# Optimization experiments

Measured on AMD Instinct MI355X. Metric: run time of the kernel, lower is better.

The kernel has to match this reference:

```python
import jax, jax.numpy as jnp
import numpy as np

EMBED_DIM = 1024
NUM_HEADS = 16
HEAD_DIM = EMBED_DIM // NUM_HEADS
BATCH = 2
SEQ = 2048


def setup_inputs() -> dict:
    key = jax.random.key(0)
    k1, k2, k3, k4, k5 = jax.random.split(key, 5)
    scale_in = 1.0 / np.sqrt(EMBED_DIM)
    return {
        "x": jax.random.normal(k1, (BATCH, SEQ, EMBED_DIM), dtype=jnp.float32),
        "head_mask": jnp.ones((NUM_HEADS,), dtype=jnp.float32),
        "qkv_w": jax.random.normal(k2, (3 * EMBED_DIM, EMBED_DIM), dtype=jnp.float32) * scale_in,
        "qkv_b": jax.random.normal(k3, (3 * EMBED_DIM,), dtype=jnp.float32) * 0.02,
        "fc_w": jax.random.normal(k4, (EMBED_DIM, EMBED_DIM), dtype=jnp.float32) * scale_in,
        "fc_b": jax.random.normal(k5, (EMBED_DIM,), dtype=jnp.float32) * 0.02,
    }


def reference(x, head_mask, qkv_w, qkv_b, fc_w, fc_b):
    N, S, D = x.shape
    H, hd = NUM_HEADS, HEAD_DIM
    # qkv Linear: y = x @ W^T + b -> [N, S, 3D]
    qkv = jnp.einsum("nsd,ed->nse", x, qkv_w) + qkv_b
    # reshape (N, S, H, 3, hd) then permute(3,0,2,1,4) -> (3, N, H, S, hd)
    qkv = qkv.reshape(N, S, H, 3, hd).transpose(3, 0, 2, 1, 4)
    q, k, v = qkv[0], qkv[1], qkv[2]
    hm = head_mask.reshape(1, H, 1, 1)
    q = q * hm
    k = k * hm
    v = v * hm
    # scores [N, H, S, S]
    energy = jnp.einsum("nhqd,nhkd->nhqk", q, k)
    attention = jax.nn.softmax(energy / jnp.sqrt(jnp.float32(hd)), axis=-1)
    out = jnp.einsum("nhqk,nhkd->nhqd", attention, v)
    out = out.transpose(0, 2, 1, 3).reshape(N, S, H * hd)
    out = jnp.einsum("nsd,ed->nse", out, fc_w) + fc_b
    return out
```

## Files before the change

### kernel.cpp

```cpp
#include <hip/hip_runtime.h>
#include <hip/hip_bf16.h>

typedef __bf16 bf16;
typedef __attribute__((ext_vector_type(8))) __bf16 bf16x8;
typedef __attribute__((ext_vector_type(4))) __bf16 bf16x4;
typedef __attribute__((ext_vector_type(4))) float f32x4;
typedef __attribute__((ext_vector_type(4))) unsigned int uint4x;

#if __has_builtin(__builtin_amdgcn_exp2f)
#define EXP2F(x) __builtin_amdgcn_exp2f(x)
#else
#define EXP2F(x) exp2f(x)
#endif

#define AS1 __attribute__((address_space(1)))
#define AS3 __attribute__((address_space(3)))

static __device__ __forceinline__ void async_ld16(const bf16* g, bf16* l) {
  __builtin_amdgcn_global_load_lds((const AS1 void*)g, (AS3 void*)l, 16, 0, 0);
}

static __device__ __forceinline__ unsigned bf16rne(float x) {
  unsigned u = __float_as_uint(x);
  return (u + 0x7fffu + ((u >> 16) & 1u)) >> 16;
}
static __device__ __forceinline__ unsigned pack2(float a, float b) {
  return bf16rne(a) | (bf16rne(b) << 16);
}

__global__ void cvt3_kernel(const float* __restrict__ x, const float* __restrict__ qw,
                            const float* __restrict__ fw, bf16* __restrict__ xb,
                            bf16* __restrict__ qwb, bf16* __restrict__ fwb) {
  int b = blockIdx.x;
  const float* src;
  bf16* dst;
  int i;
  if (b < 4096) { src = x; dst = xb; i = b * 256 + threadIdx.x; }
  else if (b < 7168) { src = qw; dst = qwb; i = (b - 4096) * 256 + threadIdx.x; }
  else { src = fw; dst = fwb; i = (b - 7168) * 256 + threadIdx.x; }
  f32x4 v = *(const f32x4*)(src + (size_t)i * 4);
  bf16x4 o;
  o[0] = (bf16)v[0]; o[1] = (bf16)v[1]; o[2] = (bf16)v[2]; o[3] = (bf16)v[3];
  *(bf16x4*)(dst + (size_t)i * 4) = o;
}

#define GEMM_STAGE(k0_, buf_)                                                    \
  {                                                                              \
    async_ld16(A + (size_t)(rowBase + r0) * Kdim + (k0_) + csw, &As[buf_][f0]);  \
    async_ld16(A + (size_t)(rowBase + r1) * Kdim + (k0_) + csw, &As[buf_][f1]);  \
    async_ld16(Bw + (size_t)(colBase + r0) * Kdim + (k0_) + csw, &Bs[buf_][f0]); \
    async_ld16(Bw + (size_t)(colBase + r1) * Kdim + (k0_) + csw, &Bs[buf_][f1]); \
  }

template <int MODE>
__global__ __launch_bounds__(256, 2) void gemm_bt_kernel(
    const bf16* __restrict__ A, const bf16* __restrict__ Bw,
    const float* __restrict__ bias, const float* __restrict__ hm,
    bf16* __restrict__ Qp, bf16* __restrict__ Kp, bf16* __restrict__ Vp,
    float* __restrict__ outF, int Ncols, int Kdim, int rowBlkCount) {
  __shared__ bf16 As[2][128 * 32];
  __shared__ bf16 Bs[2][128 * 32];
  const int t = threadIdx.x, lane = t & 63, w = t >> 6;
  const int wr = w >> 1, wc = w & 1;
  const int j = lane & 15, quad = lane >> 4;
  const int rowBlk = blockIdx.x % rowBlkCount;
  const int colBlk = blockIdx.x / rowBlkCount;
  const int rowBase = rowBlk * 128, colBase = colBlk * 128;

  f32x4 acc[4][4];
  const f32x4 z4 = {0.f, 0.f, 0.f, 0.f};
#pragma unroll
  for (int i = 0; i < 4; ++i)
#pragma unroll
    for (int jj = 0; jj < 4; ++jj) acc[i][jj] = z4;

  const int f0 = t * 8;
  const int f1 = f0 + 2048;
  const int r0 = f0 >> 5, r1 = r0 + 64;
  const int csw = (((t & 3) ^ ((r0 >> 1) & 3))) * 8;
  const int qsw = (quad ^ ((j >> 1) & 3)) * 8;

  GEMM_STAGE(0, 0);
  int buf = 0;
  for (int k0 = 0; k0 < Kdim; k0 += 32) {
    __syncthreads();
    if (k0 + 32 < Kdim) GEMM_STAGE(k0 + 32, buf ^ 1);
    bf16x8 af[4], bfr[4];
#pragma unroll
    for (int i = 0; i < 4; ++i)
      af[i] = *(const bf16x8*)&As[buf][(wr * 64 + i * 16 + j) * 32 + qsw];
#pragma unroll
    for (int jj = 0; jj < 4; ++jj)
      bfr[jj] = *(const bf16x8*)&Bs[buf][(wc * 64 + jj * 16 + j) * 32 + qsw];
#pragma unroll
    for (int i = 0; i < 4; ++i)
#pragma unroll
      for (int jj = 0; jj < 4; ++jj)
        acc[i][jj] = __builtin_amdgcn_mfma_f32_16x16x32_bf16(af[i], bfr[jj], acc[i][jj], 0, 0, 0);
    buf ^= 1;
  }

  if (MODE == 0) {
#pragma unroll
    for (int jj = 0; jj < 4; ++jj) {
      int col = colBase + wc * 64 + jj * 16 + j;
      int hh = col / 192;
      int rem = col - hh * 192;
      int mm = rem >> 6;
      int dd = rem & 63;
      float hmv = hm[hh];
      float bv = bias[col];
      float sc = (mm == 0) ? hmv * 0.18033688011112042f : hmv;
#pragma unroll
      for (int i = 0; i < 4; ++i) {
#pragma unroll
        for (int r = 0; r < 4; ++r) {
          int row = rowBase + wr * 64 + i * 16 + quad * 4 + r;
          int n = row >> 11, ss = row & 2047;
          size_t nh = (size_t)(n * 16 + hh);
          float val = (acc[i][jj][r] + bv) * sc;
          if (mm == 0) {
            Qp[nh * 131072 + ss * 64 + dd] = (bf16)val;
          } else if (mm == 1) {
            size_t idx = nh * 131072 + (size_t)(ss >> 7) * 8192 +
                         (size_t)(2 * ((ss >> 5) & 3) + ((ss >> 2) & 1)) * 1024 +
                         (dd >> 5) * 512 + ((dd >> 3) & 3) * 128 +
                         (((ss >> 3) & 3) * 4 + (ss & 3)) * 8 + (dd & 7);
            Kp[idx] = (bf16)val;
          } else {
            size_t idx = nh * 131072 + (size_t)(ss >> 7) * 8192 +
                         (((ss >> 5) & 3) * 4 + (dd >> 4)) * 512 +
                         ((ss >> 3) & 3) * 128 + (dd & 15) * 8 + (ss & 7);
            Vp[idx] = (bf16)val;
          }
        }
      }
    }
  } else {
#pragma unroll
    for (int jj = 0; jj < 4; ++jj) {
      int col = colBase + wc * 64 + jj * 16 + j;
      float bv = bias[col];
#pragma unroll
      for (int i = 0; i < 4; ++i)
#pragma unroll
        for (int r = 0; r < 4; ++r) {
          int row = rowBase + wr * 64 + i * 16 + quad * 4 + r;
          outF[(size_t)row * Ncols + col] = acc[i][jj][r] + bv;
        }
    }
  }
}

#define FLASH_STAGE(tileIdx, KsBuf, VsBuf)                                  \
  {                                                                         \
    const bf16* kn_ = Kc + (tileIdx) * 4096;                                \
    const bf16* vn_ = Vc + (tileIdx) * 4096;                                \
    _Pragma("unroll")                                                       \
    for (int p = 0; p < 2; ++p) {                                           \
      int c = (p * 256 + t) * 8;                                            \
      async_ld16(kn_ + c, &KsBuf[c]);                                       \
      async_ld16(vn_ + c, &VsBuf[c]);                                       \
    }                                                                       \
  }

#define FLASH_TILE(KsBuf, VsBuf)                                            \
  {                                                                         \
    unsigned pkd[2][4][2];                                                  \
    _Pragma("unroll")                                                       \
    for (int ct = 0; ct < 4; ++ct) {                                        \
      bf16x8 kf0 = *(const bf16x8*)&KsBuf[ct * 1024 + lane * 8];            \
      bf16x8 kf1 = *(const bf16x8*)&KsBuf[ct * 1024 + 512 + lane * 8];      \
      _Pragma("unroll")                                                     \
      for (int rt = 0; rt < 2; ++rt) {                                      \
        f32x4 sv = z4;                                                      \
        sv = __builtin_amdgcn_mfma_f32_16x16x32_bf16(kf0, qf[rt][0], sv, 0, 0, 0); \
        sv = __builtin_amdgcn_mfma_f32_16x16x32_bf16(kf1, qf[rt][1], sv, 0, 0, 0); \
        float p0 = EXP2F(sv[0]), p1 = EXP2F(sv[1]);                         \
        float p2 = EXP2F(sv[2]), p3 = EXP2F(sv[3]);                         \
        lrow[rt] += (p0 + p1) + (p2 + p3);                                  \
        pkd[rt][ct][0] = pack2(p0, p1);                                     \
        pkd[rt][ct][1] = pack2(p2, p3);                                     \
      }                                                                     \
    }                                                                       \
    _Pragma("unroll")                                                       \
    for (int kk = 0; kk < 2; ++kk) {                                        \
      union { uint4x u; bf16x8 h; } pa[2];                                  \
      _Pragma("unroll")                                                     \
      for (int rt = 0; rt < 2; ++rt)                                        \
        pa[rt].u = (uint4x){pkd[rt][2 * kk][0], pkd[rt][2 * kk][1],         \
                            pkd[rt][2 * kk + 1][0], pkd[rt][2 * kk + 1][1]};\
      _Pragma("unroll")                                                     \
      for (int dt = 0; dt < 4; ++dt) {                                      \
        bf16x8 vf = *(const bf16x8*)&VsBuf[(kk * 4 + dt) * 512 + lane * 8]; \
        oacc[0][dt] = __builtin_amdgcn_mfma_f32_16x16x32_bf16(pa[0].h, vf, oacc[0][dt], 0, 0, 0); \
        oacc[1][dt] = __builtin_amdgcn_mfma_f32_16x16x32_bf16(pa[1].h, vf, oacc[1][dt], 0, 0, 0); \
      }                                                                     \
    }                                                                       \
  }

__global__ __launch_bounds__(256, 4) void flash_kernel(const bf16* __restrict__ Qp,
                                                       const bf16* __restrict__ Kf,
                                                       const bf16* __restrict__ Vf,
                                                       float* __restrict__ O0,
                                                       float* __restrict__ O1,
                                                       float* __restrict__ Lp) {
  __shared__ bf16 Ks0[4096];
  __shared__ bf16 Vs0[4096];
  __shared__ bf16 Ks1[4096];
  __shared__ bf16 Vs1[4096];
  const int t = threadIdx.x, lane = t & 63, w = t >> 6;
  const int j = lane & 15, quad = lane >> 4;
  const int g = blockIdx.x & 63;
  const int qt = blockIdx.x >> 6;
  const int nh = g >> 1, ck = g & 1;
  const int q0 = qt * 128 + w * 32;
  const bf16* Qb = Qp + (size_t)nh * 131072;
  const bf16* Kc = Kf + (size_t)nh * 131072 + ck * 65536;
  const bf16* Vc = Vf + (size_t)nh * 131072 + ck * 65536;

  bf16x8 qf[2][2];
#pragma unroll
  for (int rt = 0; rt < 2; ++rt)
#pragma unroll
    for (int kd = 0; kd < 2; ++kd)
      qf[rt][kd] = *(const bf16x8*)&Qb[(size_t)(q0 + rt * 16 + j) * 64 + kd * 32 + quad * 8];

  float lrow[2] = {0.f, 0.f};
  f32x4 oacc[2][4];
  const f32x4 z4 = {0.f, 0.f, 0.f, 0.f};
#pragma unroll
  for (int rt = 0; rt < 2; ++rt)
#pragma unroll
    for (int dt = 0; dt < 4; ++dt) oacc[rt][dt] = z4;

  FLASH_STAGE(0, Ks0, Vs0);

  for (int it2 = 0; it2 < 8; ++it2) {
    __syncthreads();
    FLASH_STAGE(it2 * 2 + 1, Ks1, Vs1);
    FLASH_TILE(Ks0, Vs0);
    __syncthreads();
    if (it2 < 7) FLASH_STAGE(it2 * 2 + 2, Ks0, Vs0);
    FLASH_TILE(Ks1, Vs1);
  }

  float* Od = ck ? O1 : O0;
#pragma unroll
  for (int rt = 0; rt < 2; ++rt) {
    float l = lrow[rt];
    l += __shfl_xor(l, 16);
    l += __shfl_xor(l, 32);
    if (quad == 0) Lp[ck * 65536 + (size_t)nh * 2048 + q0 + rt * 16 + j] = l;
#pragma unroll
    for (int r = 0; r < 4; ++r) {
      int srow = q0 + rt * 16 + quad * 4 + r;
      size_t row = (size_t)nh * 2048 + srow;
#pragma unroll
      for (int dt = 0; dt < 4; ++dt)
        Od[row * 64 + dt * 16 + j] = oacc[rt][dt][r];
    }
  }
}

__global__ __launch_bounds__(256) void merge_kernel(const float* __restrict__ O0,
                                                    const float* __restrict__ O1,
                                                    const float* __restrict__ Lp,
                                                    bf16* __restrict__ attn) {
  int g = blockIdx.x * 256 + threadIdx.x;
  int row = g >> 4;
  int dg = (g & 15) * 4;
  float inv = 1.0f / (Lp[row] + Lp[65536 + row]);
  f32x4 a = *(const f32x4*)(O0 + (size_t)row * 64 + dg);
  f32x4 b = *(const f32x4*)(O1 + (size_t)row * 64 + dg);
  int nh = row >> 11, s = row & 2047;
  int n = nh >> 4, h = nh & 15;
  bf16x4 o;
#pragma unroll
  for (int i = 0; i < 4; ++i) o[i] = (bf16)((a[i] + b[i]) * inv);
  *(bf16x4*)(attn + ((size_t)(n * 2048 + s)) * 1024 + h * 64 + dg) = o;
}

extern "C" void kernel_launch(void* const* d_in, const int* in_sizes, int n_in,
                              void* d_out, int out_size, void* d_ws, size_t ws_size,
                              hipStream_t stream) {
  const float* x = (const float*)d_in[0];
  const float* head_mask = (const float*)d_in[1];
  const float* qkv_w = (const float*)d_in[2];
  const float* qkv_b = (const float*)d_in[3];
  const float* fc_w = (const float*)d_in[4];
  const float* fc_b = (const float*)d_in[5];
  float* out = (float*)d_out;

  char* ws = (char*)d_ws;
  bf16* x_bf    = (bf16*)(ws + 0);
  bf16* qkvw_bf = (bf16*)(ws + ((size_t)8 << 20));
  bf16* fcw_bf  = (bf16*)(ws + ((size_t)14 << 20));
  bf16* Qp      = (bf16*)(ws + ((size_t)16 << 20));
  bf16* Kf      = (bf16*)(ws + ((size_t)24 << 20));
  bf16* Vf      = (bf16*)(ws + ((size_t)32 << 20));
  float* O1     = (float*)(ws + ((size_t)40 << 20));
  float* Lp     = (float*)(ws + ((size_t)56 << 20));
  float* O0     = (float*)d_out;
  bf16* attn = x_bf;

  cvt3_kernel<<<8192, 256, 0, stream>>>(x, qkv_w, fc_w, x_bf, qkvw_bf, fcw_bf);
  gemm_bt_kernel<0><<<32 * 24, 256, 0, stream>>>(x_bf, qkvw_bf, qkv_b, head_mask,
                                                 Qp, Kf, Vf, nullptr, 3072, 1024, 32);
  flash_kernel<<<1024, 256, 0, stream>>>(Qp, Kf, Vf, O0, O1, Lp);
  merge_kernel<<<4096, 256, 0, stream>>>(O0, O1, Lp, attn);
  gemm_bt_kernel<1><<<32 * 8, 256, 0, stream>>>(attn, fcw_bf, fc_b, nullptr,
                                                nullptr, nullptr, nullptr, out, 1024, 1024, 32);
}
```

Measured before the change: 203.1 us.

## Fuse split-K attention halves within one block and drop merge kernel

The two key-range halves for each query tile, which used to be separate blocks writing fp32 partial outputs and row sums to global memory, now run as two 256-thread halves of one 512-thread block. The halves combine their partial outputs and row sums through shared memory and write normalized bf16 attention output directly. This removes the separate merge kernel launch and the global round trip of fp32 partials. In exchange the block is twice as large, needs twice the LDS for staging plus a reduction buffer, and the grid is halved, which can lower occupancy.

```diff
diff --git a/kernel.cpp b/kernel.cpp
--- a/kernel.cpp
+++ b/kernel.cpp
@@ -158,9 +158,9 @@
     const bf16* vn_ = Vc + (tileIdx) * 4096;                                \
     _Pragma("unroll")                                                       \
     for (int p = 0; p < 2; ++p) {                                           \
-      int c = (p * 256 + t) * 8;                                            \
-      async_ld16(kn_ + c, &KsBuf[c]);                                       \
-      async_ld16(vn_ + c, &VsBuf[c]);                                       \
+      int c = (p * 256 + ts) * 8;                                           \
+      async_ld16(kn_ + c, &(KsBuf)[c]);                                     \
+      async_ld16(vn_ + c, &(VsBuf)[c]);                                     \
     }                                                                       \
   }
 
@@ -169,8 +169,8 @@
     unsigned pkd[2][4][2];                                                  \
     _Pragma("unroll")                                                       \
     for (int ct = 0; ct < 4; ++ct) {                                        \
-      bf16x8 kf0 = *(const bf16x8*)&KsBuf[ct * 1024 + lane * 8];            \
-      bf16x8 kf1 = *(const bf16x8*)&KsBuf[ct * 1024 + 512 + lane * 8];      \
+      bf16x8 kf0 = *(const bf16x8*)&(KsBuf)[ct * 1024 + lane * 8];          \
+      bf16x8 kf1 = *(const bf16x8*)&(KsBuf)[ct * 1024 + 512 + lane * 8];    \
       _Pragma("unroll")                                                     \
       for (int rt = 0; rt < 2; ++rt) {                                      \
         f32x4 sv = z4;                                                      \
@@ -192,32 +192,31 @@
                             pkd[rt][2 * kk + 1][0], pkd[rt][2 * kk + 1][1]};\
       _Pragma("unroll")                                                     \
       for (int dt = 0; dt < 4; ++dt) {                                      \
-        bf16x8 vf = *(const bf16x8*)&VsBuf[(kk * 4 + dt) * 512 + lane * 8]; \
+        bf16x8 vf = *(const bf16x8*)&(VsBuf)[(kk * 4 + dt) * 512 + lane * 8]; \
         oacc[0][dt] = __builtin_amdgcn_mfma_f32_16x16x32_bf16(pa[0].h, vf, oacc[0][dt], 0, 0, 0); \
         oacc[1][dt] = __builtin_amdgcn_mfma_f32_16x16x32_bf16(pa[1].h, vf, oacc[1][dt], 0, 0, 0); \
       }                                                                     \
     }                                                                       \
   }
 
-__global__ __launch_bounds__(256, 4) void flash_kernel(const bf16* __restrict__ Qp,
+__global__ __launch_bounds__(512, 4) void flash_kernel(const bf16* __restrict__ Qp,
                                                        const bf16* __restrict__ Kf,
                                                        const bf16* __restrict__ Vf,
-                                                       float* __restrict__ O0,
-                                                       float* __restrict__ O1,
-                                                       float* __restrict__ Lp) {
-  __shared__ bf16 Ks0[4096];
-  __shared__ bf16 Vs0[4096];
-  __shared__ bf16 Ks1[4096];
-  __shared__ bf16 Vs1[4096];
+                                                       bf16* __restrict__ attn) {
+  __shared__ bf16 Kst[2][2][4096];
+  __shared__ bf16 Vst[2][2][4096];
+  __shared__ float Lsh[8][32];
   const int t = threadIdx.x, lane = t & 63, w = t >> 6;
+  const int ts = t & 255;
+  const int hc = t >> 8;
   const int j = lane & 15, quad = lane >> 4;
-  const int g = blockIdx.x & 63;
-  const int qt = blockIdx.x >> 6;
-  const int nh = g >> 1, ck = g & 1;
-  const int q0 = qt * 128 + w * 32;
+  const int b = blockIdx.x;
+  const int qt = b >> 5;
+  const int nh = b & 31;
+  const int q0 = qt * 128 + (w & 3) * 32;
   const bf16* Qb = Qp + (size_t)nh * 131072;
-  const bf16* Kc = Kf + (size_t)nh * 131072 + ck * 65536;
-  const bf16* Vc = Vf + (size_t)nh * 131072 + ck * 65536;
+  const bf16* Kc = Kf + (size_t)nh * 131072 + hc * 65536;
+  const bf16* Vc = Vf + (size_t)nh * 131072 + hc * 65536;
 
   bf16x8 qf[2][2];
 #pragma unroll
@@ -234,51 +233,66 @@
 #pragma unroll
     for (int dt = 0; dt < 4; ++dt) oacc[rt][dt] = z4;
 
-  FLASH_STAGE(0, Ks0, Vs0);
+  FLASH_STAGE(0, Kst[hc][0], Vst[hc][0]);
 
   for (int it2 = 0; it2 < 8; ++it2) {
     __syncthreads();
-    FLASH_STAGE(it2 * 2 + 1, Ks1, Vs1);
-    FLASH_TILE(Ks0, Vs0);
+    FLASH_STAGE(it2 * 2 + 1, Kst[hc][1], Vst[hc][1]);
+    FLASH_TILE(Kst[hc][0], Vst[hc][0]);
     __syncthreads();
-    if (it2 < 7) FLASH_STAGE(it2 * 2 + 2, Ks0, Vs0);
-    FLASH_TILE(Ks1, Vs1);
-  }
-
-  float* Od = ck ? O1 : O0;
+    if (it2 < 7) FLASH_STAGE(it2 * 2 + 2, Kst[hc][0], Vst[hc][0]);
+    FLASH_TILE(Kst[hc][1], Vst[hc][1]);
+  }
+
+  float lf[2];
 #pragma unroll
   for (int rt = 0; rt < 2; ++rt) {
     float l = lrow[rt];
     l += __shfl_xor(l, 16);
     l += __shfl_xor(l, 32);
-    if (quad == 0) Lp[ck * 65536 + (size_t)nh * 2048 + q0 + rt * 16 + j] = l;
-#pragma unroll
-    for (int r = 0; r < 4; ++r) {
-      int srow = q0 + rt * 16 + quad * 4 + r;
-      size_t row = (size_t)nh * 2048 + srow;
+    lf[rt] = l;
+  }
+  __syncthreads();
+  if (quad == 0) {
+    Lsh[w][j] = lf[0];
+    Lsh[w][16 + j] = lf[1];
+  }
+  float* Osh = (float*)&Kst[0][0][0];
+  if (w >= 4) {
+    int wb = w - 4;
+#pragma unroll
+    for (int rt = 0; rt < 2; ++rt)
 #pragma unroll
       for (int dt = 0; dt < 4; ++dt)
-        Od[row * 64 + dt * 16 + j] = oacc[rt][dt][r];
-    }
-  }
-}
-
-__global__ __launch_bounds__(256) void merge_kernel(const float* __restrict__ O0,
-                                                    const float* __restrict__ O1,
-                                                    const float* __restrict__ Lp,
-                                                    bf16* __restrict__ attn) {
-  int g = blockIdx.x * 256 + threadIdx.x;
-  int row = g >> 4;
-  int dg = (g & 15) * 4;
-  float inv = 1.0f / (Lp[row] + Lp[65536 + row]);
-  f32x4 a = *(const f32x4*)(O0 + (size_t)row * 64 + dg);
-  f32x4 b = *(const f32x4*)(O1 + (size_t)row * 64 + dg);
-  int nh = row >> 11, s = row & 2047;
-  int n = nh >> 4, h = nh & 15;
-  bf16x4 o;
-#pragma unroll
-  for (int i = 0; i < 4; ++i) o[i] = (bf16)((a[i] + b[i]) * inv);
-  *(bf16x4*)(attn + ((size_t)(n * 2048 + s)) * 1024 + h * 64 + dg) = o;
+#pragma unroll
+        for (int r = 0; r < 4; ++r)
+          Osh[((((wb * 2 + rt) * 4 + dt) * 4) + r) * 64 + lane] = oacc[rt][dt][r];
+  }
+  __syncthreads();
+  if (w < 4) {
+    int n = nh >> 4, h = nh & 15;
+    float inv[2][4];
+#pragma unroll
+    for (int rt = 0; rt < 2; ++rt)
+#pragma unroll
+      for (int r = 0; r < 4; ++r) {
+        int idx = rt * 16 + quad * 4 + r;
+        inv[rt][r] = 1.0f / (Lsh[w][idx] + Lsh[w + 4][idx]);
+      }
+#pragma unroll
+    for (int rt = 0; rt < 2; ++rt)
+#pragma unroll
+      for (int r = 0; r < 4; ++r) {
+        int s = q0 + rt * 16 + quad * 4 + r;
+        size_t base = ((size_t)(n * 2048 + s)) * 1024 + h * 64;
+#pragma unroll
+        for (int dt = 0; dt < 4; ++dt) {
+          float o = oacc[rt][dt][r] +
+                    Osh[((((w * 2 + rt) * 4 + dt) * 4) + r) * 64 + lane];
+          attn[base + dt * 16 + j] = (bf16)(o * inv[rt][r]);
+        }
+      }
+  }
 }
 
 extern "C" void kernel_launch(void* const* d_in, const int* in_sizes, int n_in,
@@ -299,16 +313,12 @@
   bf16* Qp      = (bf16*)(ws + ((size_t)16 << 20));
   bf16* Kf      = (bf16*)(ws + ((size_t)24 << 20));
   bf16* Vf      = (bf16*)(ws + ((size_t)32 << 20));
-  float* O1     = (float*)(ws + ((size_t)40 << 20));
-  float* Lp     = (float*)(ws + ((size_t)56 << 20));
-  float* O0     = (float*)d_out;
   bf16* attn = x_bf;
 
   cvt3_kernel<<<8192, 256, 0, stream>>>(x, qkv_w, fc_w, x_bf, qkvw_bf, fcw_bf);
   gemm_bt_kernel<0><<<32 * 24, 256, 0, stream>>>(x_bf, qkvw_bf, qkv_b, head_mask,
                                                  Qp, Kf, Vf, nullptr, 3072, 1024, 32);
-  flash_kernel<<<1024, 256, 0, stream>>>(Qp, Kf, Vf, O0, O1, Lp);
-  merge_kernel<<<4096, 256, 0, stream>>>(O0, O1, Lp, attn);
+  flash_kernel<<<512, 512, 0, stream>>>(Qp, Kf, Vf, attn);
   gemm_bt_kernel<1><<<32 * 8, 256, 0, stream>>>(attn, fcw_bf, fc_b, nullptr,
                                                 nullptr, nullptr, nullptr, out, 1024, 1024, 32);
 }
```

New measurement: 191.3 us. -5.8%, faster.
